# Kernel optimization log

Measured on AMD Instinct MI355X. Metric: run time of the kernel, lower is better.

## Reference

```python
import jax, jax.numpy as jnp
import numpy as np

N_NODES = 10000
N_EDGES = 300000
NUM_HIDDEN = 256
NUM_IN = 512
NUM_HEADS = 4


def _lin(key, fin, fout):
    kw, kb = jax.random.split(key)
    w = jax.random.normal(kw, (fin, fout), dtype=jnp.float32) * (1.0 / np.sqrt(fin))
    b = jax.random.normal(kb, (fout,), dtype=jnp.float32) * 0.01
    return w, b


def setup_inputs() -> dict:
    key = jax.random.key(0)
    ks = jax.random.split(key, 12)
    h_V = jax.random.normal(ks[0], (N_NODES, NUM_HIDDEN), dtype=jnp.float32)
    h_E = jax.random.normal(ks[1], (N_EDGES, NUM_IN), dtype=jnp.float32)
    center_id = jnp.sort(jax.random.randint(ks[2], (N_EDGES,), 0, N_NODES, dtype=jnp.int32))
    batch_id = jax.random.randint(ks[3], (N_EDGES,), 0, 8, dtype=jnp.int32)
    # W_V: Linear(num_in, H) -> GELU -> Linear(H, H) -> GELU -> Linear(H, H)
    wv1_w, wv1_b = _lin(ks[4], NUM_IN, NUM_HIDDEN)
    wv2_w, wv2_b = _lin(ks[5], NUM_HIDDEN, NUM_HIDDEN)
    wv3_w, wv3_b = _lin(ks[6], NUM_HIDDEN, NUM_HIDDEN)
    # Bias: Linear(3H, H) -> ReLU -> Linear(H, H) -> ReLU -> Linear(H, num_heads)
    b1_w, b1_b = _lin(ks[7], 3 * NUM_HIDDEN, NUM_HIDDEN)
    b2_w, b2_b = _lin(ks[8], NUM_HIDDEN, NUM_HIDDEN)
    b3_w, b3_b = _lin(ks[9], NUM_HIDDEN, NUM_HEADS)
    # W_O: Linear(H, H, bias=False)
    wo_w, _ = _lin(ks[10], NUM_HIDDEN, NUM_HIDDEN)
    return {
        "h_V": h_V, "h_E": h_E,
        "wv1_w": wv1_w, "wv1_b": wv1_b, "wv2_w": wv2_w, "wv2_b": wv2_b,
        "wv3_w": wv3_w, "wv3_b": wv3_b,
        "b1_w": b1_w, "b1_b": b1_b, "b2_w": b2_w, "b2_b": b2_b,
        "b3_w": b3_w, "b3_b": b3_b,
        "wo_w": wo_w,
        "center_id": center_id, "batch_id": batch_id,
    }


def reference(h_V, h_E, wv1_w, wv1_b, wv2_w, wv2_b, wv3_w, wv3_b,
              b1_w, b1_b, b2_w, b2_b, b3_w, b3_b, wo_w,
              center_id, batch_id):
    N = h_V.shape[0]
    E = h_E.shape[0]
    n_heads = NUM_HEADS
    d = h_V.shape[1] // n_heads  # head dim

    # Bias MLP on gathered center node feats concat edge feats -> per-edge, per-head logit
    x = jnp.concatenate([h_V[center_id], h_E], axis=-1)  # [E, 3H]
    x = jax.nn.relu(x @ b1_w + b1_b)
    x = jax.nn.relu(x @ b2_w + b2_b)
    w = x @ b3_w + b3_b                                   # [E, n_heads]
    logits = w / np.float32(np.sqrt(d))

    # W_V MLP (exact GELU, matching torch nn.GELU default)
    v = jax.nn.gelu(h_E @ wv1_w + wv1_b, approximate=False)
    v = jax.nn.gelu(v @ wv2_w + wv2_b, approximate=False)
    v = (v @ wv3_w + wv3_b).reshape(E, n_heads, d)        # [E, n_heads, d]

    # scatter_softmax over edges sharing the same center node
    seg_max = jax.ops.segment_max(logits, center_id, num_segments=N)  # [N, n_heads]
    p = jnp.exp(logits - seg_max[center_id])                          # [E, n_heads]
    denom = jax.ops.segment_sum(p, center_id, num_segments=N)         # [N, n_heads]
    attend = p / denom[center_id]                                     # [E, n_heads]

    # weighted scatter-sum of values
    out = jax.ops.segment_sum(attend[:, :, None] * v, center_id, num_segments=N)
    out = out.reshape(N, n_heads * d)                                 # [N, H]
    return out @ wo_w
```

## Files before the change

kernel.cpp:

```cpp
#include <hip/hip_runtime.h>
#include <hip/hip_bf16.h>
#include <math.h>

#define H 256
#define NIN 512
#define NHEADS 4
#define BM 64
#define LOG2E 1.4426950408889634f

typedef __attribute__((ext_vector_type(8))) short short8;
typedef __attribute__((ext_vector_type(4))) short short4v;
typedef __attribute__((ext_vector_type(4))) float floatx4;

__device__ __forceinline__ float4 ld4(const float* p){ return *reinterpret_cast<const float4*>(p); }

__device__ __forceinline__ short f2bf(float x){
    __hip_bfloat16 h = __float2bfloat16(x);
    return *reinterpret_cast<short*>(&h);
}
__device__ __forceinline__ float bf2f(short h){
    return __uint_as_float(((unsigned)(unsigned short)h) << 16);
}
__device__ __forceinline__ float fexp2(float x){ return __builtin_amdgcn_exp2f(x); }
__device__ __forceinline__ float frcp(float x){ return __builtin_amdgcn_rcpf(x); }

__device__ __forceinline__ float gelu_fast(float x){
    float y = x * fmaf(x*x, 0.0356774081f, 0.7978845608f);
    float t = fexp2(-2.8853900818f * fabsf(y));
    float th = (1.f - t) * frcp(1.f + t);
    th = copysignf(th, y);
    return 0.5f * x * (1.f + th);
}
__device__ __forceinline__ floatx4 mfma16(short8 a, short8 b, floatx4 c){
    return __builtin_amdgcn_mfma_f32_16x16x32_bf16(a, b, c, 0, 0, 0);
}
__device__ __forceinline__ short8 pack8(float4 a, float4 b){
    short8 v;
    v[0]=f2bf(a.x); v[1]=f2bf(a.y); v[2]=f2bf(a.z); v[3]=f2bf(a.w);
    v[4]=f2bf(b.x); v[5]=f2bf(b.y); v[6]=f2bf(b.z); v[7]=f2bf(b.w);
    return v;
}

#define ZERO_ACC() do { \
    _Pragma("unroll") \
    for (int i_=0;i_<4;i_++){ \
        _Pragma("unroll") \
        for (int j_=0;j_<4;j_++) acc[i_][j_] = (floatx4){0.f,0.f,0.f,0.f}; \
    } \
} while(0)

#define LOADB(DST, WF, NCH, CH) do { \
    _Pragma("unroll") \
    for (int s_=0;s_<2;s_++) \
        _Pragma("unroll") \
        for (int n_=0;n_<4;n_++) \
            DST[s_][n_] = *reinterpret_cast<const short8*>( \
                &(WF)[(size_t)((((w*4+n_)*(NCH) + (CH))*2 + s_) << 9) + lane*8]); \
} while(0)

#define COPYB(DST, SRC) do { \
    _Pragma("unroll") \
    for (int s_=0;s_<2;s_++) \
        _Pragma("unroll") \
        for (int n_=0;n_<4;n_++) DST[s_][n_] = SRC[s_][n_]; \
} while(0)

#define MFMA_LDS(BC, ABASE, ASTR) do { \
    _Pragma("unroll") \
    for (int s_=0;s_<2;s_++){ \
        short8 af_[4]; \
        _Pragma("unroll") \
        for (int rb_=0;rb_<4;rb_++) \
            af_[rb_] = *reinterpret_cast<const short8*>( \
                &(ABASE)[(rb_*16+lr)*(ASTR) + s_*32 + lh*8]); \
        _Pragma("unroll") \
        for (int n_=0;n_<4;n_++) \
            _Pragma("unroll") \
            for (int rb_=0;rb_<4;rb_++) \
                acc[rb_][n_] = mfma16(af_[rb_], BC[s_][n_], acc[rb_][n_]); \
    } \
} while(0)

__global__ void k_ranges(const int* __restrict__ center, int* __restrict__ start, int E, int N)
{
    int n = blockIdx.x*blockDim.x + threadIdx.x;
    if (n > N) return;
    if (n == N){ start[N] = E; return; }
    int lo = 0, hi = E;
    while (lo < hi){ int mid = (lo+hi)>>1; if (center[mid] < n) lo = mid+1; else hi = mid; }
    start[n] = lo;
}

__global__ void __launch_bounds__(256)
k_wconvf(const float* __restrict__ src, short* __restrict__ dst, int KK)
{
    const int cb = blockIdx.x;
    const int ch = blockIdx.y;
    const int NCH = KK >> 6;
    const int t = threadIdx.x;
    const int s = t >> 7;
    const int rem = t & 127;
    const int ln = rem >> 1;
    const int j0 = (rem & 1) * 4;
    const int k = ch*64 + s*32 + ((ln>>4)<<3) + j0;
    const int col = cb*16 + (ln & 15);
    short4v o;
    o[0] = f2bf(src[(size_t)(k+0)*H + col]);
    o[1] = f2bf(src[(size_t)(k+1)*H + col]);
    o[2] = f2bf(src[(size_t)(k+2)*H + col]);
    o[3] = f2bf(src[(size_t)(k+3)*H + col]);
    *reinterpret_cast<short4v*>(&dst[(size_t)(((cb*NCH + ch)*2 + s) << 9) + ln*8 + j0]) = o;
}

__global__ void k_w3padf(const float* __restrict__ b3w, short* __restrict__ dst)
{
    const int t = threadIdx.x;
    const int ch = t >> 6, ln = t & 63;
    const int col = ln & 15;
    #pragma unroll
    for (int s=0;s<2;s++){
        #pragma unroll
        for (int j=0;j<8;j++){
            int k = ch*64 + s*32 + ((ln>>4)<<3) + j;
            dst[((ch*2 + s) << 9) + ln*8 + j] =
                (col < NHEADS) ? f2bf(b3w[(size_t)k*NHEADS + col]) : (short)0;
        }
    }
}

__global__ void __launch_bounds__(256)
k_nodebias(const float* __restrict__ hV, const float* __restrict__ b1w,
           const float* __restrict__ b1b, float* __restrict__ nb, int N)
{
    __shared__ float ps[8][260];
    const int n0 = blockIdx.x*8;
    const int tid = threadIdx.x;
    {
        int r = tid >> 5, cq = (tid & 31)*8;
        *reinterpret_cast<float4*>(&ps[r][cq])   = ld4(&hV[(size_t)(n0+r)*H + cq]);
        *reinterpret_cast<float4*>(&ps[r][cq+4]) = ld4(&hV[(size_t)(n0+r)*H + cq + 4]);
    }
    __syncthreads();
    float a[8];
    float bias = b1b[tid];
    #pragma unroll
    for (int i=0;i<8;i++) a[i] = bias;
    #pragma unroll 4
    for (int k=0;k<H;k++){
        float w = b1w[(size_t)k*H + tid];
        #pragma unroll
        for (int i=0;i<8;i++) a[i] = fmaf(ps[i][k], w, a[i]);
    }
    #pragma unroll
    for (int i=0;i<8;i++) nb[(size_t)(n0+i)*H + tid] = a[i];
}

__global__ void __launch_bounds__(256,3)
k_bias2(const float* __restrict__ hE,
        const short* __restrict__ Wf1,
        const short* __restrict__ Wf2,
        const short* __restrict__ W3f,
        const float* __restrict__ b3b,
        const float* __restrict__ b2b,
        const float* __restrict__ nodebias,
        const int* __restrict__ center,
        float* __restrict__ logits, int E)
{
    __shared__ short Alds[2][BM][72];
    __shared__ short xarena[BM][264];
    __shared__ int   csh[BM];

    const int tid = threadIdx.x;
    const int lane = tid & 63, w = tid >> 6;
    const int lr = lane & 15, lh = lane >> 4;
    const int e0 = blockIdx.x * BM;
    const int srow = tid >> 2, skq = tid & 3;
    const int gsrow = (e0 + srow < E) ? (e0 + srow) : (E-1);
    const float* aSrc = hE + (size_t)gsrow * NIN + skq * 16;

    if (tid < BM){ int ge = e0 + tid; csh[tid] = center[ge < E ? ge : E-1]; }

    floatx4 acc[4][4];
    ZERO_ACC();

    short8 bc[2][4], bn[2][4];
    LOADB(bc, Wf1, 8, 0);
    float4 pf[4];
    #pragma unroll
    for (int q=0;q<4;q++) pf[q] = ld4(aSrc + q*4);
    *reinterpret_cast<short8*>(&Alds[0][srow][skq*16])   = pack8(pf[0], pf[1]);
    *reinterpret_cast<short8*>(&Alds[0][srow][skq*16+8]) = pack8(pf[2], pf[3]);
    __syncthreads();

    #pragma unroll
    for (int ch = 0; ch < 8; ch++){
        if (ch < 7){
            LOADB(bn, Wf1, 8, ch+1);
            #pragma unroll
            for (int q=0;q<4;q++) pf[q] = ld4(aSrc + (ch+1)*64 + q*4);
        }
        __builtin_amdgcn_s_setprio(1);
        MFMA_LDS(bc, &Alds[ch&1][0][0], 72);
        __builtin_amdgcn_s_setprio(0);
        if (ch < 7){
            *reinterpret_cast<short8*>(&Alds[(ch&1)^1][srow][skq*16])   = pack8(pf[0], pf[1]);
            *reinterpret_cast<short8*>(&Alds[(ch&1)^1][srow][skq*16+8]) = pack8(pf[2], pf[3]);
            COPYB(bc, bn);
        }
        __syncthreads();
    }
    const int c0 = w * 64;
    #pragma unroll
    for (int rb=0;rb<4;rb++)
        #pragma unroll
        for (int j=0;j<4;j++){
            const int row = rb*16 + lh*4 + j;
            const float* nb = nodebias + (size_t)csh[row]*H + c0 + lr;
            #pragma unroll
            for (int n=0;n<4;n++)
                xarena[row][c0 + n*16 + lr] = f2bf(fmaxf(acc[rb][n][j] + nb[n*16], 0.f));
        }
    __syncthreads();

    ZERO_ACC();
    LOADB(bc, Wf2, 4, 0);
    #pragma unroll
    for (int ch = 0; ch < 4; ch++){
        if (ch < 3) LOADB(bn, Wf2, 4, ch+1);
        __builtin_amdgcn_s_setprio(1);
        MFMA_LDS(bc, &xarena[0][ch*64], 264);
        __builtin_amdgcn_s_setprio(0);
        if (ch < 3) COPYB(bc, bn);
    }
    float bb[4];
    #pragma unroll
    for (int n=0;n<4;n++) bb[n] = b2b[c0 + n*16 + lr];
    __syncthreads();
    #pragma unroll
    for (int rb=0;rb<4;rb++)
        #pragma unroll
        for (int j=0;j<4;j++){
            const int row = rb*16 + lh*4 + j;
            #pragma unroll
            for (int n=0;n<4;n++)
                xarena[row][c0 + n*16 + lr] = f2bf(fmaxf(acc[rb][n][j] + bb[n], 0.f));
        }
    __syncthreads();

    floatx4 a3[4];
    #pragma unroll
    for (int rb=0;rb<4;rb++) a3[rb] = (floatx4){0.f,0.f,0.f,0.f};
    short8 b3fr[4][2];
    #pragma unroll
    for (int ch=0;ch<4;ch++)
        #pragma unroll
        for (int s=0;s<2;s++)
            b3fr[ch][s] = *reinterpret_cast<const short8*>(&W3f[((ch*2+s)<<9) + lane*8]);
    #pragma unroll
    for (int ch=0;ch<4;ch++)
        #pragma unroll
        for (int s=0;s<2;s++)
            #pragma unroll
            for (int rb=0;rb<4;rb++){
                short8 af = *reinterpret_cast<const short8*>(&xarena[rb*16+lr][ch*64 + s*32 + lh*8]);
                a3[rb] = mfma16(af, b3fr[ch][s], a3[rb]);
            }
    if (w == 0 && lr < NHEADS){
        float bias = b3b[lr];
        #pragma unroll
        for (int rb=0;rb<4;rb++)
            #pragma unroll
            for (int j=0;j<4;j++){
                int ge = e0 + rb*16 + lh*4 + j;
                if (ge < E) logits[(size_t)ge*NHEADS + lr] = (a3[rb][j] + bias) * 0.125f;
            }
    }
}

__global__ void k_smstats(const float* __restrict__ logits, const int* __restrict__ start,
                          float* __restrict__ mbuf, float* __restrict__ dbuf)
{
    int n = blockIdx.x;
    int s = start[n], e_end = start[n+1];
    int lane = threadIdx.x;
    int i = lane >> 2, hh = lane & 3;
    float mx = -INFINITY;
    for (int b = s + i; b < e_end; b += 16) mx = fmaxf(mx, logits[(size_t)b*NHEADS + hh]);
    #pragma unroll
    for (int off=4; off<64; off<<=1) mx = fmaxf(mx, __shfl_xor(mx, off, 64));
    float sum = 0.f;
    for (int b = s + i; b < e_end; b += 16) sum += expf(logits[(size_t)b*NHEADS + hh] - mx);
    #pragma unroll
    for (int off=4; off<64; off<<=1) sum += __shfl_xor(sum, off, 64);
    if (lane < 4){ mbuf[(size_t)n*NHEADS + hh] = mx; dbuf[(size_t)n*NHEADS + hh] = sum; }
}

__global__ void __launch_bounds__(256,3)
k_wv2(const float* __restrict__ hE,
      const short* __restrict__ Wf1, const float* __restrict__ b1v,
      const short* __restrict__ Wf2, const float* __restrict__ b2v,
      const short* __restrict__ Wf3, const float* __restrict__ b3v,
      const int* __restrict__ center, const float* __restrict__ logits,
      const float* __restrict__ mbuf, const float* __restrict__ dbuf,
      float* __restrict__ pre, int E)
{
    __shared__ short Alds[2][BM][72];
    __shared__ short xarena[BM][264];
    __shared__ int   csh[BM];

    const int tid = threadIdx.x;
    const int lane = tid & 63, w = tid >> 6;
    const int lr = lane & 15, lh = lane >> 4;
    const int e0 = blockIdx.x * BM;
    const int srow = tid >> 2, skq = tid & 3;
    const int gsrow = (e0 + srow < E) ? (e0 + srow) : (E-1);
    const float* aSrc = hE + (size_t)gsrow * NIN + skq * 16;

    if (tid < BM){ int ge = e0 + tid; csh[tid] = center[ge < E ? ge : E-1]; }

    floatx4 acc[4][4];
    ZERO_ACC();

    short8 bc[2][4], bn[2][4];
    LOADB(bc, Wf1, 8, 0);
    float4 pf[4];
    #pragma unroll
    for (int q=0;q<4;q++) pf[q] = ld4(aSrc + q*4);
    *reinterpret_cast<short8*>(&Alds[0][srow][skq*16])   = pack8(pf[0], pf[1]);
    *reinterpret_cast<short8*>(&Alds[0][srow][skq*16+8]) = pack8(pf[2], pf[3]);
    __syncthreads();

    #pragma unroll
    for (int ch = 0; ch < 8; ch++){
        if (ch < 7){
            LOADB(bn, Wf1, 8, ch+1);
            #pragma unroll
            for (int q=0;q<4;q++) pf[q] = ld4(aSrc + (ch+1)*64 + q*4);
        }
        __builtin_amdgcn_s_setprio(1);
        MFMA_LDS(bc, &Alds[ch&1][0][0], 72);
        __builtin_amdgcn_s_setprio(0);
        if (ch < 7){
            *reinterpret_cast<short8*>(&Alds[(ch&1)^1][srow][skq*16])   = pack8(pf[0], pf[1]);
            *reinterpret_cast<short8*>(&Alds[(ch&1)^1][srow][skq*16+8]) = pack8(pf[2], pf[3]);
            COPYB(bc, bn);
        }
        __syncthreads();
    }
    const int c0 = w * 64;
    {
        float bcv[4];
        #pragma unroll
        for (int n=0;n<4;n++) bcv[n] = b1v[c0 + n*16 + lr];
        #pragma unroll
        for (int rb=0;rb<4;rb++)
            #pragma unroll
            for (int j=0;j<4;j++){
                const int row = rb*16 + lh*4 + j;
                #pragma unroll
                for (int n=0;n<4;n++)
                    xarena[row][c0 + n*16 + lr] = f2bf(gelu_fast(acc[rb][n][j] + bcv[n]));
            }
    }
    __syncthreads();

    ZERO_ACC();
    LOADB(bc, Wf2, 4, 0);
    #pragma unroll
    for (int ch = 0; ch < 4; ch++){
        if (ch < 3) LOADB(bn, Wf2, 4, ch+1);
        __builtin_amdgcn_s_setprio(1);
        MFMA_LDS(bc, &xarena[0][ch*64], 264);
        __builtin_amdgcn_s_setprio(0);
        if (ch < 3) COPYB(bc, bn);
    }
    float bc2[4];
    #pragma unroll
    for (int n=0;n<4;n++) bc2[n] = b2v[c0 + n*16 + lr];
    __syncthreads();
    #pragma unroll
    for (int rb=0;rb<4;rb++)
        #pragma unroll
        for (int j=0;j<4;j++){
            const int row = rb*16 + lh*4 + j;
            #pragma unroll
            for (int n=0;n<4;n++)
                xarena[row][c0 + n*16 + lr] = f2bf(gelu_fast(acc[rb][n][j] + bc2[n]));
        }
    __syncthreads();

    ZERO_ACC();
    LOADB(bc, Wf3, 4, 0);
    #pragma unroll
    for (int ch = 0; ch < 4; ch++){
        if (ch < 3) LOADB(bn, Wf3, 4, ch+1);
        __builtin_amdgcn_s_setprio(1);
        MFMA_LDS(bc, &xarena[0][ch*64], 264);
        __builtin_amdgcn_s_setprio(0);
        if (ch < 3) COPYB(bc, bn);
    }
    float bc3[4];
    #pragma unroll
    for (int n=0;n<4;n++) bc3[n] = b3v[c0 + n*16 + lr];
    __syncthreads();

    #pragma unroll
    for (int rb=0;rb<4;rb++)
        #pragma unroll
        for (int j=0;j<4;j++){
            const int row = rb*16 + lh*4 + j;
            const int ge = e0 + row;
            float att = 0.f;
            if (ge < E){
                const int c = csh[row];
                att = fexp2((logits[(size_t)ge*NHEADS + w] - mbuf[(size_t)c*NHEADS + w]) * LOG2E)
                      * frcp(dbuf[(size_t)c*NHEADS + w]);
            }
            #pragma unroll
            for (int n=0;n<4;n++)
                xarena[row][c0 + n*16 + lr] = f2bf((acc[rb][n][j] + bc3[n]) * att);
        }
    __syncthreads();
    {
        const int col = tid;
        float s = 0.f; int cur = csh[0];
        for (int e=0;e<BM;e++){
            int c = csh[e];
            if (c != cur){ atomicAdd(&pre[(size_t)cur*H + col], s); s = 0.f; cur = c; }
            s += bf2f(xarena[e][col]);
        }
        atomicAdd(&pre[(size_t)cur*H + col], s);
    }
}

__global__ void __launch_bounds__(256)
k_out(const float* __restrict__ pre, const float* __restrict__ wo,
      float* __restrict__ out, int N)
{
    __shared__ float ps[8][260];
    const int tid = threadIdx.x;
    const int nb = blockIdx.x * 8;
    {
        int r = tid >> 5, c = (tid & 31) * 8;
        *reinterpret_cast<float4*>(&ps[r][c])   = ld4(&pre[(size_t)(nb+r)*H + c]);
        *reinterpret_cast<float4*>(&ps[r][c+4]) = ld4(&pre[(size_t)(nb+r)*H + c+4]);
    }
    __syncthreads();
    float a[8];
    #pragma unroll
    for (int i=0;i<8;i++) a[i]=0.f;
    #pragma unroll 4
    for (int k=0;k<H;k++){
        float w = wo[(size_t)k*H + tid];
        #pragma unroll
        for (int i=0;i<8;i++) a[i] = fmaf(ps[i][k], w, a[i]);
    }
    #pragma unroll
    for (int i=0;i<8;i++)
        out[(size_t)(nb+i)*H + tid] = a[i];
}

extern "C" void kernel_launch(void* const* d_in, const int* in_sizes, int n_in,
                              void* d_out, int out_size, void* d_ws, size_t ws_size,
                              hipStream_t stream)
{
    const float* hV   = (const float*)d_in[0];
    const float* hE   = (const float*)d_in[1];
    const float* wv1w = (const float*)d_in[2];
    const float* wv1b = (const float*)d_in[3];
    const float* wv2w = (const float*)d_in[4];
    const float* wv2b = (const float*)d_in[5];
    const float* wv3w = (const float*)d_in[6];
    const float* wv3b = (const float*)d_in[7];
    const float* b1w  = (const float*)d_in[8];
    const float* b1b  = (const float*)d_in[9];
    const float* b2w  = (const float*)d_in[10];
    const float* b2b  = (const float*)d_in[11];
    const float* b3w  = (const float*)d_in[12];
    const float* b3b  = (const float*)d_in[13];
    const float* wow  = (const float*)d_in[14];
    const int*   center = (const int*)d_in[15];

    const int E = in_sizes[15];
    const int N = in_sizes[0] / H;
    const int nblk = (E + BM - 1) / BM;

    float* pre      = (float*)d_ws;
    float* logits   = pre + (size_t)N*H;
    float* mbuf     = logits + (size_t)E*NHEADS;
    float* dbuf     = mbuf + (size_t)N*NHEADS;
    int*   start    = (int*)(dbuf + (size_t)N*NHEADS);
    float* nodebias = (float*)(start + ((N+1+3)&~3));
    short* wf1b     = (short*)(nodebias + (size_t)N*H);
    short* wf2b     = wf1b + 512*256;
    short* w3fb     = wf2b + 256*256;
    short* wf1v     = w3fb + 16*256;
    short* wf2v     = wf1v + 512*256;
    short* wf3v     = wf2v + 256*256;

    hipMemsetAsync(pre, 0, (size_t)N*H*sizeof(float), stream);
    k_ranges<<<(N+1+255)/256, 256, 0, stream>>>(center, start, E, N);
    k_wconvf<<<dim3(16,8), 256, 0, stream>>>(b1w + 256*H, wf1b, 512);
    k_wconvf<<<dim3(16,4), 256, 0, stream>>>(b2w,  wf2b, 256);
    k_w3padf<<<1, 256, 0, stream>>>(b3w, w3fb);
    k_wconvf<<<dim3(16,8), 256, 0, stream>>>(wv1w, wf1v, 512);
    k_wconvf<<<dim3(16,4), 256, 0, stream>>>(wv2w, wf2v, 256);
    k_wconvf<<<dim3(16,4), 256, 0, stream>>>(wv3w, wf3v, 256);
    k_nodebias<<<N/8, 256, 0, stream>>>(hV, b1w, b1b, nodebias, N);
    k_bias2<<<nblk, 256, 0, stream>>>(hE, wf1b, wf2b, w3fb, b3b, b2b, nodebias, center, logits, E);
    k_smstats<<<N, 64, 0, stream>>>(logits, start, mbuf, dbuf);
    k_wv2<<<nblk, 256, 0, stream>>>(hE, wf1v, wv1b, wf2v, wv2b, wf3v, wv3b,
                                    center, logits, mbuf, dbuf, pre, E);
    k_out<<<N/8, 256, 0, stream>>>(pre, wow, (float*)d_out, N);
}
```

Measured before the change: 638.8 us.

## Cache bf16 copy of h_E in bias kernel and read it directly in W_V kernel

The bias kernel now writes a bf16 copy of h_E to workspace while it stages the tile, and the W_V kernel loads its A fragments from that bf16 buffer straight from global memory instead of re-reading fp32 h_E through LDS with per-chunk barriers. This halves the second read of the large edge-feature tensor and removes the LDS staging and syncs in the first GEMM of k_wv2, at the cost of an extra bf16 write (~300MB→150MB) in k_bias2. The final head projection in k_bias2 is also split across the four waves instead of being done redundantly by all of them.

New measurement: 771.7 us. +20.8%, slower.

```diff
diff --git a/kernel.cpp b/kernel.cpp
--- a/kernel.cpp
+++ b/kernel.cpp
@@ -73,6 +73,22 @@
         for (int rb_=0;rb_<4;rb_++) \
             af_[rb_] = *reinterpret_cast<const short8*>( \
                 &(ABASE)[(rb_*16+lr)*(ASTR) + s_*32 + lh*8]); \
+        _Pragma("unroll") \
+        for (int n_=0;n_<4;n_++) \
+            _Pragma("unroll") \
+            for (int rb_=0;rb_<4;rb_++) \
+                acc[rb_][n_] = mfma16(af_[rb_], BC[s_][n_], acc[rb_][n_]); \
+    } \
+} while(0)
+
+#define MFMA_GLB(BC, CH) do { \
+    _Pragma("unroll") \
+    for (int s_=0;s_<2;s_++){ \
+        short8 af_[4]; \
+        _Pragma("unroll") \
+        for (int rb_=0;rb_<4;rb_++) \
+            af_[rb_] = *reinterpret_cast<const short8*>( \
+                arow[rb_] + (CH)*64 + s_*32 + lh*8); \
         _Pragma("unroll") \
         for (int n_=0;n_<4;n_++) \
             _Pragma("unroll") \
@@ -164,7 +180,8 @@
         const float* __restrict__ b2b,
         const float* __restrict__ nodebias,
         const int* __restrict__ center,
-        float* __restrict__ logits, int E)
+        float* __restrict__ logits,
+        short* __restrict__ hEb, int E)
 {
     __shared__ short Alds[2][BM][72];
     __shared__ short xarena[BM][264];
@@ -177,6 +194,7 @@
     const int srow = tid >> 2, skq = tid & 3;
     const int gsrow = (e0 + srow < E) ? (e0 + srow) : (E-1);
     const float* aSrc = hE + (size_t)gsrow * NIN + skq * 16;
+    short* ebDst = hEb + (size_t)gsrow * NIN + skq * 16;
 
     if (tid < BM){ int ge = e0 + tid; csh[tid] = center[ge < E ? ge : E-1]; }
 
@@ -188,8 +206,13 @@
     float4 pf[4];
     #pragma unroll
     for (int q=0;q<4;q++) pf[q] = ld4(aSrc + q*4);
-    *reinterpret_cast<short8*>(&Alds[0][srow][skq*16])   = pack8(pf[0], pf[1]);
-    *reinterpret_cast<short8*>(&Alds[0][srow][skq*16+8]) = pack8(pf[2], pf[3]);
+    {
+        short8 s8a = pack8(pf[0], pf[1]), s8b = pack8(pf[2], pf[3]);
+        *reinterpret_cast<short8*>(&Alds[0][srow][skq*16])   = s8a;
+        *reinterpret_cast<short8*>(&Alds[0][srow][skq*16+8]) = s8b;
+        *reinterpret_cast<short8*>(ebDst)     = s8a;
+        *reinterpret_cast<short8*>(ebDst + 8) = s8b;
+    }
     __syncthreads();
 
     #pragma unroll
@@ -203,8 +226,11 @@
         MFMA_LDS(bc, &Alds[ch&1][0][0], 72);
         __builtin_amdgcn_s_setprio(0);
         if (ch < 7){
-            *reinterpret_cast<short8*>(&Alds[(ch&1)^1][srow][skq*16])   = pack8(pf[0], pf[1]);
-            *reinterpret_cast<short8*>(&Alds[(ch&1)^1][srow][skq*16+8]) = pack8(pf[2], pf[3]);
+            short8 s8a = pack8(pf[0], pf[1]), s8b = pack8(pf[2], pf[3]);
+            *reinterpret_cast<short8*>(&Alds[(ch&1)^1][srow][skq*16])   = s8a;
+            *reinterpret_cast<short8*>(&Alds[(ch&1)^1][srow][skq*16+8]) = s8b;
+            *reinterpret_cast<short8*>(ebDst + (ch+1)*64)     = s8a;
+            *reinterpret_cast<short8*>(ebDst + (ch+1)*64 + 8) = s8b;
             COPYB(bc, bn);
         }
         __syncthreads();
@@ -247,33 +273,22 @@
         }
     __syncthreads();
 
-    floatx4 a3[4];
-    #pragma unroll
-    for (int rb=0;rb<4;rb++) a3[rb] = (floatx4){0.f,0.f,0.f,0.f};
-    short8 b3fr[4][2];
+    floatx4 a3 = (floatx4){0.f,0.f,0.f,0.f};
     #pragma unroll
     for (int ch=0;ch<4;ch++)
         #pragma unroll
-        for (int s=0;s<2;s++)
-            b3fr[ch][s] = *reinterpret_cast<const short8*>(&W3f[((ch*2+s)<<9) + lane*8]);
-    #pragma unroll
-    for (int ch=0;ch<4;ch++)
-        #pragma unroll
-        for (int s=0;s<2;s++)
-            #pragma unroll
-            for (int rb=0;rb<4;rb++){
-                short8 af = *reinterpret_cast<const short8*>(&xarena[rb*16+lr][ch*64 + s*32 + lh*8]);
-                a3[rb] = mfma16(af, b3fr[ch][s], a3[rb]);
-            }
-    if (w == 0 && lr < NHEADS){
+        for (int s=0;s<2;s++){
+            short8 bfr = *reinterpret_cast<const short8*>(&W3f[((ch*2+s)<<9) + lane*8]);
+            short8 af = *reinterpret_cast<const short8*>(&xarena[w*16+lr][ch*64 + s*32 + lh*8]);
+            a3 = mfma16(af, bfr, a3);
+        }
+    if (lr < NHEADS){
         float bias = b3b[lr];
         #pragma unroll
-        for (int rb=0;rb<4;rb++)
-            #pragma unroll
-            for (int j=0;j<4;j++){
-                int ge = e0 + rb*16 + lh*4 + j;
-                if (ge < E) logits[(size_t)ge*NHEADS + lr] = (a3[rb][j] + bias) * 0.125f;
-            }
+        for (int j=0;j<4;j++){
+            int ge = e0 + w*16 + lh*4 + j;
+            if (ge < E) logits[(size_t)ge*NHEADS + lr] = (a3[j] + bias) * 0.125f;
+        }
     }
 }
 
@@ -296,7 +311,7 @@
 }
 
 __global__ void __launch_bounds__(256,3)
-k_wv2(const float* __restrict__ hE,
+k_wv2(const short* __restrict__ hEb,
       const short* __restrict__ Wf1, const float* __restrict__ b1v,
       const short* __restrict__ Wf2, const float* __restrict__ b2v,
       const short* __restrict__ Wf3, const float* __restrict__ b3v,
@@ -304,7 +319,6 @@
       const float* __restrict__ mbuf, const float* __restrict__ dbuf,
       float* __restrict__ pre, int E)
 {
-    __shared__ short Alds[2][BM][72];
     __shared__ short xarena[BM][264];
     __shared__ int   csh[BM];
 
@@ -312,42 +326,32 @@
     const int lane = tid & 63, w = tid >> 6;
     const int lr = lane & 15, lh = lane >> 4;
     const int e0 = blockIdx.x * BM;
-    const int srow = tid >> 2, skq = tid & 3;
-    const int gsrow = (e0 + srow < E) ? (e0 + srow) : (E-1);
-    const float* aSrc = hE + (size_t)gsrow * NIN + skq * 16;
 
     if (tid < BM){ int ge = e0 + tid; csh[tid] = center[ge < E ? ge : E-1]; }
+
+    const short* arow[4];
+    #pragma unroll
+    for (int rb=0;rb<4;rb++){
+        int r = e0 + rb*16 + lr; if (r >= E) r = E-1;
+        arow[rb] = hEb + (size_t)r*NIN;
+    }
 
     floatx4 acc[4][4];
     ZERO_ACC();
 
     short8 bc[2][4], bn[2][4];
     LOADB(bc, Wf1, 8, 0);
-    float4 pf[4];
-    #pragma unroll
-    for (int q=0;q<4;q++) pf[q] = ld4(aSrc + q*4);
-    *reinterpret_cast<short8*>(&Alds[0][srow][skq*16])   = pack8(pf[0], pf[1]);
-    *reinterpret_cast<short8*>(&Alds[0][srow][skq*16+8]) = pack8(pf[2], pf[3]);
-    __syncthreads();
 
     #pragma unroll
     for (int ch = 0; ch < 8; ch++){
-        if (ch < 7){
-            LOADB(bn, Wf1, 8, ch+1);
-            #pragma unroll
-            for (int q=0;q<4;q++) pf[q] = ld4(aSrc + (ch+1)*64 + q*4);
-        }
+        if (ch < 7) LOADB(bn, Wf1, 8, ch+1);
         __builtin_amdgcn_s_setprio(1);
-        MFMA_LDS(bc, &Alds[ch&1][0][0], 72);
+        MFMA_GLB(bc, ch);
         __builtin_amdgcn_s_setprio(0);
-        if (ch < 7){
-            *reinterpret_cast<short8*>(&Alds[(ch&1)^1][srow][skq*16])   = pack8(pf[0], pf[1]);
-            *reinterpret_cast<short8*>(&Alds[(ch&1)^1][srow][skq*16+8]) = pack8(pf[2], pf[3]);
-            COPYB(bc, bn);
-        }
-        __syncthreads();
+        if (ch < 7) COPYB(bc, bn);
     }
     const int c0 = w * 64;
+    __syncthreads();
     {
         float bcv[4];
         #pragma unroll
@@ -497,6 +501,7 @@
     short* wf1v     = w3fb + 16*256;
     short* wf2v     = wf1v + 512*256;
     short* wf3v     = wf2v + 256*256;
+    short* hEb      = wf3v + 256*256;
 
     hipMemsetAsync(pre, 0, (size_t)N*H*sizeof(float), stream);
     k_ranges<<<(N+1+255)/256, 256, 0, stream>>>(center, start, E, N);
@@ -507,9 +512,10 @@
     k_wconvf<<<dim3(16,4), 256, 0, stream>>>(wv2w, wf2v, 256);
     k_wconvf<<<dim3(16,4), 256, 0, stream>>>(wv3w, wf3v, 256);
     k_nodebias<<<N/8, 256, 0, stream>>>(hV, b1w, b1b, nodebias, N);
-    k_bias2<<<nblk, 256, 0, stream>>>(hE, wf1b, wf2b, w3fb, b3b, b2b, nodebias, center, logits, E);
+    k_bias2<<<nblk, 256, 0, stream>>>(hE, wf1b, wf2b, w3fb, b3b, b2b, nodebias, center,
+                                      logits, hEb, E);
     k_smstats<<<N, 64, 0, stream>>>(logits, start, mbuf, dbuf);
-    k_wv2<<<nblk, 256, 0, stream>>>(hE, wf1v, wv1b, wf2v, wv2b, wf3v, wv3b,
+    k_wv2<<<nblk, 256, 0, stream>>>(hEb, wf1v, wv1b, wf2v, wv2b, wf3v, wv3b,
                                     center, logits, mbuf, dbuf, pre, E);
     k_out<<<N/8, 256, 0, stream>>>(pre, wow, (float*)d_out, N);
 }
```
